# Performance work log

Hardware: AMD Instinct MI355X
Metric: run time of the kernel (lower is better)

## Reference

```python
import jax, jax.numpy as jnp
import numpy as np


def setup_inputs() -> dict:
    key = jax.random.key(0)
    k1, k2 = jax.random.split(key)
    B, C, H, W = 8, 64, 64, 64
    x = jax.random.normal(k1, (B, C, H, W), dtype=jnp.float32)
    stdv = 1.0 / np.sqrt(C)
    weight = jax.random.uniform(k2, (C, C), dtype=jnp.float32, minval=-stdv, maxval=stdv)
    return {"x": x, "weight": weight}


def reference(x, weight):
    B, C, H, W = x.shape
    N = H * W
    xf = x.reshape(B, C, N)            # [B, C, N]
    g_x = jnp.transpose(xf, (0, 2, 1))  # [B, N, C] (also theta_x)
    # f[b, i, j] = sum_c x[b, c, i] * x[b, c, j]
    f = jnp.einsum('bic,bcj->bij', g_x, xf)  # [B, N, N]
    adj = jax.nn.softmax(f, axis=-1)
    support = jnp.einsum('bnc,cd->bnd', g_x, weight)  # [B, N, C]
    y = jnp.einsum('bij,bjc->bic', adj, support)      # [B, N, C]
    y = jnp.transpose(y, (0, 2, 1)).reshape(B, C, H, W)
    return y + x
```

## Files before the change

### kernel.cpp

```cpp
#include <hip/hip_runtime.h>
#include <stdint.h>


#define NTOK 4096
#define CCH  64

typedef float v4f __attribute__((ext_vector_type(4)));
typedef __bf16 v8bf __attribute__((ext_vector_type(8)));
typedef unsigned short v8us __attribute__((ext_vector_type(8)));
typedef __fp16 v2fp __attribute__((ext_vector_type(2)));
typedef _Float16 v8h __attribute__((ext_vector_type(8)));

__device__ __forceinline__ unsigned short f2bf(float f) {
    union { float f; unsigned int u; } c; c.f = f;
    unsigned int r = c.u + 0x7fffu + ((c.u >> 16) & 1u);
    return (unsigned short)(r >> 16);
}

__device__ __forceinline__ v8bf ld8(const unsigned short* p) {
    union { v8us s; v8bf b; } u;
    u.s = *(const v8us*)p;
    return u.b;
}

__device__ __forceinline__ unsigned int pkbf(float a, float b) {
    union { float f; unsigned int u; } ua, ub; ua.f = a; ub.f = b;
    return __builtin_amdgcn_perm(ub.u, ua.u, 0x07060302u);
}

__device__ __forceinline__ float ex2(float x) {
#if __has_builtin(__builtin_amdgcn_exp2f)
    return __builtin_amdgcn_exp2f(x);
#else
    return exp2f(x);
#endif
}

__device__ __forceinline__ void gload_lds16(const void* g, void* l) {
    __builtin_amdgcn_global_load_lds(
        (const __attribute__((address_space(1))) unsigned int*)g,
        (__attribute__((address_space(3))) unsigned int*)l,
        16, 0, 0);
}

__global__ __launch_bounds__(256) void prep_kernel(
    const float* __restrict__ x,
    const float* __restrict__ w,
    unsigned short* __restrict__ xT,
    unsigned short* __restrict__ sT)
{
    __shared__ float Xf[64 * 65];

    const int tid  = threadIdx.x;
    const int lane = tid & 63;
    const int wv   = __builtin_amdgcn_readfirstlane(tid >> 6);
    const int b    = blockIdx.y;
    const int n0   = blockIdx.x * 64;

    const float* xb = x + (size_t)b * CCH * NTOK + n0 + lane;
    #pragma unroll
    for (int k = 0; k < 16; ++k) {
        const int c = wv * 16 + k;
        Xf[c * 65 + lane] = xb[(size_t)c * NTOK];
    }
    __syncthreads();

    {
        const int n  = tid >> 2;
        const int c0 = (tid & 3) * 16;
        unsigned int pk[8];
        #pragma unroll
        for (int k = 0; k < 8; ++k) {
            const float a = Xf[(c0 + 2 * k) * 65 + n];
            const float c2 = Xf[(c0 + 2 * k + 1) * 65 + n];
            pk[k] = (unsigned int)f2bf(a) | ((unsigned int)f2bf(c2) << 16);
        }
        unsigned short* xtr = xT + ((size_t)b * NTOK + n0 + n) * CCH + c0;
        *(uint4*)(xtr)     = *(uint4*)(pk);
        *(uint4*)(xtr + 8) = *(uint4*)(pk + 4);
    }

    float acc[16];
    #pragma unroll
    for (int d = 0; d < 16; ++d) acc[d] = 0.f;

    #pragma unroll 4
    for (int c = 0; c < 64; ++c) {
        const float xc = Xf[c * 65 + lane];
        const float* wr = w + c * 64 + wv * 16;
        #pragma unroll
        for (int d = 0; d < 16; ++d) acc[d] = fmaf(xc, wr[d], acc[d]);
    }
    unsigned short* stb = sT + (size_t)b * CCH * NTOK + n0 + lane;
    #pragma unroll
    for (int d = 0; d < 16; ++d)
        stb[(size_t)(wv * 16 + d) * NTOK] = f2bf(acc[d]);
}

__global__ __launch_bounds__(256, 4) void flash_kernel(
    const unsigned short* __restrict__ xT,
    const unsigned short* __restrict__ sT,
    unsigned short* __restrict__ part_o,
    float* __restrict__ part_l,
    int nchunk, int chunk_len)
{
    __shared__ __align__(16) unsigned short Kt[2][64 * 64];
    __shared__ __align__(16) unsigned short Vt[2][64 * 64];

    const int tid  = threadIdx.x;
    const int w    = tid >> 6;
    const int lane = tid & 63;
    const int quad = lane >> 4;
    const int l16  = lane & 15;
    const int b     = blockIdx.z;
    const int chunk = blockIdx.y;
    const int i0   = blockIdx.x * 128;
    const int irow = i0 + w * 32;
    const int jb   = chunk * chunk_len;

    const unsigned short* xTb = xT + (size_t)b * NTOK * CCH;
    const unsigned short* sTb = sT + (size_t)b * CCH * NTOK;

    const int srow = w * 8 + (lane >> 3);
    const int sc   = (lane & 7) ^ (lane >> 3);
    const int ksrow = 8 * ((srow & 12) >> 2) + 4 * ((srow >> 4) & 1) + (srow & 3);

    auto stage = [&](int j0, int bf) {
        unsigned short* kd = Kt[bf] + w * 512;
        unsigned short* vd = Vt[bf] + w * 512;
        gload_lds16(xTb + (size_t)(j0 + ksrow) * CCH + sc * 8,       kd);
        gload_lds16(xTb + (size_t)(j0 + 32 + ksrow) * CCH + sc * 8,  kd + 2048);
        gload_lds16(sTb + (size_t)srow * NTOK + j0 + sc * 8,        vd);
        gload_lds16(sTb + (size_t)(32 + srow) * NTOK + j0 + sc * 8, vd + 2048);
    };

    stage(jb, 0);

    v8bf aq0[2], aq1[2];
    #pragma unroll
    for (int m = 0; m < 2; ++m) {
        const unsigned short* qr = xTb + (size_t)(irow + m * 16 + l16) * CCH + quad * 8;
        aq0[m] = ld8(qr);
        aq1[m] = ld8(qr + 32);
    }

    const float L2E = 1.4426950408889634f;
    float negm2[2];
    #pragma unroll
    for (int m = 0; m < 2; ++m) {
        float msq = 0.f;
        #pragma unroll
        for (int i = 0; i < 8; ++i) {
            float e0 = (float)aq0[m][i], e1 = (float)aq1[m][i];
            msq = fmaf(e0, e0, msq);
            msq = fmaf(e1, e1, msq);
        }
        msq += __shfl_xor(msq, 16);
        msq += __shfl_xor(msq, 32);
        negm2[m] = -msq * L2E;
    }

    v4f o[2][4];
    #pragma unroll
    for (int m = 0; m < 2; ++m)
        #pragma unroll
        for (int ct = 0; ct < 4; ++ct) { o[m][ct][0]=0.f; o[m][ct][1]=0.f; o[m][ct][2]=0.f; o[m][ct][3]=0.f; }
    float rsum[2] = {0.f, 0.f};

    int cur = 0;
    for (int jj = 0; jj < chunk_len; jj += 64) {
        __syncthreads();
        if (jj + 64 < chunk_len)
            stage(jb + jj + 64, cur ^ 1);

        const unsigned short* Kc = Kt[cur];
        const unsigned short* Vc = Vt[cur];

        #pragma unroll
        for (int h = 0; h < 2; ++h) {
            uint2 pk[2][2];
            #pragma unroll
            for (int jtl = 0; jtl < 2; ++jtl) {
                const int krow = 32 * h + 16 * jtl + l16;
                const unsigned short* kb = Kc + krow * 64;
                const int c0 = quad ^ (krow & 7);
                v8bf bk0 = ld8(kb + c0 * 8);
                v8bf bk1 = ld8(kb + (c0 ^ 4) * 8);
                #pragma unroll
                for (int m = 0; m < 2; ++m) {
                    v4f z; z[0]=0.f; z[1]=0.f; z[2]=0.f; z[3]=0.f;
                    z = __builtin_amdgcn_mfma_f32_16x16x32_bf16(bk0, aq0[m], z, 0, 0, 0);
                    z = __builtin_amdgcn_mfma_f32_16x16x32_bf16(bk1, aq1[m], z, 0, 0, 0);
                    const float p0 = ex2(fmaf(z[0], L2E, negm2[m]));
                    const float p1 = ex2(fmaf(z[1], L2E, negm2[m]));
                    const float p2 = ex2(fmaf(z[2], L2E, negm2[m]));
                    const float p3 = ex2(fmaf(z[3], L2E, negm2[m]));
                    rsum[m] += (p0 + p1) + (p2 + p3);
                    pk[m][jtl].x = pkbf(p0, p1);
                    pk[m][jtl].y = pkbf(p2, p3);
                }
            }

            union { unsigned int u[4]; v8bf b; } pb[2];
            #pragma unroll
            for (int m = 0; m < 2; ++m) {
                pb[m].u[0] = pk[m][0].x; pb[m].u[1] = pk[m][0].y;
                pb[m].u[2] = pk[m][1].x; pb[m].u[3] = pk[m][1].y;
            }

            #pragma unroll
            for (int ct = 0; ct < 4; ++ct) {
                const int vrow = 16 * ct + l16;
                const unsigned short* vb = Vc + vrow * 64;
                const int cc = (4 * h + quad) ^ (vrow & 7);
                v8bf bv = ld8(vb + cc * 8);
                #pragma unroll
                for (int m = 0; m < 2; ++m)
                    o[m][ct] = __builtin_amdgcn_mfma_f32_16x16x32_bf16(bv, pb[m].b, o[m][ct], 0, 0, 0);
            }
        }
        cur ^= 1;
    }

    const size_t pbase = (size_t)(b * nchunk + chunk) * NTOK + irow;
    #pragma unroll
    for (int m = 0; m < 2; ++m) {
        float t = rsum[m];
        t += __shfl_xor(t, 16);
        t += __shfl_xor(t, 32);
        if (quad == 0) part_l[pbase + m * 16 + l16] = t;
    }
    unsigned short* po = part_o + pbase * 64;
    #pragma unroll
    for (int m = 0; m < 2; ++m)
        #pragma unroll
        for (int ct = 0; ct < 4; ++ct) {
            union { struct { v2fp a, b; } h; uint2 u; } cv;
            cv.h.a = __builtin_amdgcn_cvt_pkrtz(o[m][ct][0], o[m][ct][1]);
            cv.h.b = __builtin_amdgcn_cvt_pkrtz(o[m][ct][2], o[m][ct][3]);
            *(uint2*)(po + (size_t)(m * 16 + l16) * 64 + ct * 16 + quad * 4) = cv.u;
        }
}

__global__ __launch_bounds__(256) void combine_kernel(
    const unsigned short* __restrict__ part_o,
    const float* __restrict__ part_l,
    const float* __restrict__ x,
    float* __restrict__ out,
    int nchunk)
{
    __shared__ float Of[64 * 65];
    const int tid = threadIdx.x;
    const int b = blockIdx.y;
    const int i0 = blockIdx.x * 64;
    const int row = tid >> 2;
    const int seg = tid & 3;

    float acc[16];
    #pragma unroll
    for (int k = 0; k < 16; ++k) acc[k] = 0.f;
    float lt = 0.f;

    auto body = [&](int ch) {
        const size_t base = (size_t)(b * nchunk + ch) * NTOK + i0 + row;
        lt += part_l[base];
        const unsigned short* po = part_o + base * 64 + seg * 16;
        v8h a = *(const v8h*)(po);
        v8h c2 = *(const v8h*)(po + 8);
        #pragma unroll
        for (int k = 0; k < 8; ++k) {
            acc[k]     += (float)a[k];
            acc[8 + k] += (float)c2[k];
        }
    };
    if (nchunk == 4) { body(0); body(1); body(2); body(3); }
    else { for (int ch = 0; ch < nchunk; ++ch) body(ch); }

    const float inv = 1.f / lt;
    #pragma unroll
    for (int k = 0; k < 16; ++k) Of[row * 65 + seg * 16 + k] = acc[k] * inv;
    __syncthreads();

    const int c    = tid >> 2;
    const int part = tid & 3;
    const float* xrow = x   + ((size_t)b * CCH + c) * NTOK + i0 + part * 16;
    float*       orow = out + ((size_t)b * CCH + c) * NTOK + i0 + part * 16;
    #pragma unroll
    for (int i4 = 0; i4 < 4; ++i4) {
        float4 xv = *(const float4*)(xrow + i4 * 4);
        float4 ov;
        ov.x = Of[(part * 16 + i4 * 4 + 0) * 65 + c] + xv.x;
        ov.y = Of[(part * 16 + i4 * 4 + 1) * 65 + c] + xv.y;
        ov.z = Of[(part * 16 + i4 * 4 + 2) * 65 + c] + xv.z;
        ov.w = Of[(part * 16 + i4 * 4 + 3) * 65 + c] + xv.w;
        *(float4*)(orow + i4 * 4) = ov;
    }
}

extern "C" void kernel_launch(void* const* d_in, const int* in_sizes, int n_in,
                              void* d_out, int out_size, void* d_ws, size_t ws_size,
                              hipStream_t stream) {
    const float* x = (const float*)d_in[0];
    const float* w = (const float*)d_in[1];
    float* out = (float*)d_out;

    const size_t xT_elems = (size_t)8 * NTOK * CCH;
    unsigned short* xT = (unsigned short*)d_ws;
    unsigned short* sT = xT + xT_elems;
    char* rest = (char*)d_ws + 2 * xT_elems * sizeof(unsigned short);

    int KS = 4;
    while (KS > 1) {
        size_t need = 2 * xT_elems * sizeof(unsigned short)
                    + (size_t)KS * ((size_t)8 * NTOK * CCH * 2 + (size_t)8 * NTOK * 4);
        if (need <= ws_size) break;
        KS >>= 1;
    }
    unsigned short* part_o = (unsigned short*)rest;
    float* part_l = (float*)(rest + (size_t)KS * 8 * NTOK * CCH * 2);

    dim3 gp(64, 8);
    prep_kernel<<<gp, 256, 0, stream>>>(x, w, xT, sT);
    dim3 gf(32, KS, 8);
    flash_kernel<<<gf, 256, 0, stream>>>(xT, sT, part_o, part_l, KS, NTOK / KS);
    dim3 gc(64, 8);
    combine_kernel<<<gc, 256, 0, stream>>>(part_o, part_l, x, out, KS);
}
```

Before: 119.3 us.

## Fuse split-K combine into flash kernel via last-block atomic counter

Removes the separate combine kernel launch. Each flash block increments a per-tile atomic counter after writing its partials, and the last-arriving chunk block reduces all partials, normalises, adds the residual and writes the output. The shared memory for the K/V tiles is reused for the transpose buffer. The counters are zeroed in the prep kernel. This saves a launch and its tail, but the reduction now runs only on the last blocks, which can lengthen the flash kernel's tail.

```diff
diff --git a/kernel.cpp b/kernel.cpp
--- a/kernel.cpp
+++ b/kernel.cpp
@@ -47,7 +47,8 @@
     const float* __restrict__ x,
     const float* __restrict__ w,
     unsigned short* __restrict__ xT,
-    unsigned short* __restrict__ sT)
+    unsigned short* __restrict__ sT,
+    int* __restrict__ cnt)
 {
     __shared__ float Xf[64 * 65];
 
@@ -57,6 +58,9 @@
     const int b    = blockIdx.y;
     const int n0   = blockIdx.x * 64;
 
+    if (blockIdx.x == 0 && blockIdx.y == 0)
+        cnt[tid] = 0;
+
     const float* xb = x + (size_t)b * CCH * NTOK + n0 + lane;
     #pragma unroll
     for (int k = 0; k < 16; ++k) {
@@ -102,10 +106,15 @@
     const unsigned short* __restrict__ sT,
     unsigned short* __restrict__ part_o,
     float* __restrict__ part_l,
+    const float* __restrict__ x,
+    float* __restrict__ out,
+    int* __restrict__ cnt,
     int nchunk, int chunk_len)
 {
-    __shared__ __align__(16) unsigned short Kt[2][64 * 64];
-    __shared__ __align__(16) unsigned short Vt[2][64 * 64];
+    __shared__ __align__(16) unsigned char smem[32768];
+    __shared__ int s_last;
+    unsigned short* KT = (unsigned short*)smem;
+    unsigned short* VT = KT + 2 * 4096;
 
     const int tid  = threadIdx.x;
     const int w    = tid >> 6;
@@ -126,8 +135,8 @@
     const int ksrow = 8 * ((srow & 12) >> 2) + 4 * ((srow >> 4) & 1) + (srow & 3);
 
     auto stage = [&](int j0, int bf) {
-        unsigned short* kd = Kt[bf] + w * 512;
-        unsigned short* vd = Vt[bf] + w * 512;
+        unsigned short* kd = KT + bf * 4096 + w * 512;
+        unsigned short* vd = VT + bf * 4096 + w * 512;
         gload_lds16(xTb + (size_t)(j0 + ksrow) * CCH + sc * 8,       kd);
         gload_lds16(xTb + (size_t)(j0 + 32 + ksrow) * CCH + sc * 8,  kd + 2048);
         gload_lds16(sTb + (size_t)srow * NTOK + j0 + sc * 8,        vd);
@@ -173,8 +182,8 @@
         if (jj + 64 < chunk_len)
             stage(jb + jj + 64, cur ^ 1);
 
-        const unsigned short* Kc = Kt[cur];
-        const unsigned short* Vc = Vt[cur];
+        const unsigned short* Kc = KT + cur * 4096;
+        const unsigned short* Vc = VT + cur * 4096;
 
         #pragma unroll
         for (int h = 0; h < 2; ++h) {
@@ -240,60 +249,65 @@
             cv.h.b = __builtin_amdgcn_cvt_pkrtz(o[m][ct][2], o[m][ct][3]);
             *(uint2*)(po + (size_t)(m * 16 + l16) * 64 + ct * 16 + quad * 4) = cv.u;
         }
-}
-
-__global__ __launch_bounds__(256) void combine_kernel(
-    const unsigned short* __restrict__ part_o,
-    const float* __restrict__ part_l,
-    const float* __restrict__ x,
-    float* __restrict__ out,
-    int nchunk)
-{
-    __shared__ float Of[64 * 65];
-    const int tid = threadIdx.x;
-    const int b = blockIdx.y;
-    const int i0 = blockIdx.x * 64;
+
+    __threadfence();
+    __syncthreads();
+    if (tid == 0)
+        s_last = (atomicAdd(&cnt[b * 32 + blockIdx.x], 1) == nchunk - 1);
+    __syncthreads();
+    if (!s_last) return;
+    __threadfence();
+
+    float* Of = (float*)smem;
     const int row = tid >> 2;
     const int seg = tid & 3;
-
-    float acc[16];
-    #pragma unroll
-    for (int k = 0; k < 16; ++k) acc[k] = 0.f;
-    float lt = 0.f;
-
-    auto body = [&](int ch) {
-        const size_t base = (size_t)(b * nchunk + ch) * NTOK + i0 + row;
-        lt += part_l[base];
-        const unsigned short* po = part_o + base * 64 + seg * 16;
-        v8h a = *(const v8h*)(po);
-        v8h c2 = *(const v8h*)(po + 8);
-        #pragma unroll
-        for (int k = 0; k < 8; ++k) {
-            acc[k]     += (float)a[k];
-            acc[8 + k] += (float)c2[k];
-        }
-    };
-    if (nchunk == 4) { body(0); body(1); body(2); body(3); }
-    else { for (int ch = 0; ch < nchunk; ++ch) body(ch); }
-
-    const float inv = 1.f / lt;
-    #pragma unroll
-    for (int k = 0; k < 16; ++k) Of[row * 65 + seg * 16 + k] = acc[k] * inv;
-    __syncthreads();
-
     const int c    = tid >> 2;
     const int part = tid & 3;
-    const float* xrow = x   + ((size_t)b * CCH + c) * NTOK + i0 + part * 16;
-    float*       orow = out + ((size_t)b * CCH + c) * NTOK + i0 + part * 16;
-    #pragma unroll
-    for (int i4 = 0; i4 < 4; ++i4) {
-        float4 xv = *(const float4*)(xrow + i4 * 4);
-        float4 ov;
-        ov.x = Of[(part * 16 + i4 * 4 + 0) * 65 + c] + xv.x;
-        ov.y = Of[(part * 16 + i4 * 4 + 1) * 65 + c] + xv.y;
-        ov.z = Of[(part * 16 + i4 * 4 + 2) * 65 + c] + xv.z;
-        ov.w = Of[(part * 16 + i4 * 4 + 3) * 65 + c] + xv.w;
-        *(float4*)(orow + i4 * 4) = ov;
+    const float* xb2  = x   + (size_t)b * CCH * NTOK;
+    float*       outb = out + (size_t)b * CCH * NTOK;
+
+    #pragma unroll
+    for (int g = 0; g < 2; ++g) {
+        const int r0 = i0 + g * 64;
+
+        float acc[16];
+        #pragma unroll
+        for (int k = 0; k < 16; ++k) acc[k] = 0.f;
+        float lt = 0.f;
+
+        auto body = [&](int ch) {
+            const size_t base = (size_t)(b * nchunk + ch) * NTOK + r0 + row;
+            lt += part_l[base];
+            const unsigned short* pp = part_o + base * 64 + seg * 16;
+            v8h a  = *(const v8h*)(pp);
+            v8h c2 = *(const v8h*)(pp + 8);
+            #pragma unroll
+            for (int k = 0; k < 8; ++k) {
+                acc[k]     += (float)a[k];
+                acc[8 + k] += (float)c2[k];
+            }
+        };
+        if (nchunk == 4) { body(0); body(1); body(2); body(3); }
+        else { for (int ch = 0; ch < nchunk; ++ch) body(ch); }
+
+        const float inv = 1.f / lt;
+        #pragma unroll
+        for (int k = 0; k < 16; ++k) Of[row * 65 + seg * 16 + k] = acc[k] * inv;
+        __syncthreads();
+
+        const float* xrow = xb2  + (size_t)c * NTOK + r0 + part * 16;
+        float*       orow = outb + (size_t)c * NTOK + r0 + part * 16;
+        #pragma unroll
+        for (int i4 = 0; i4 < 4; ++i4) {
+            float4 xv = *(const float4*)(xrow + i4 * 4);
+            float4 ov;
+            ov.x = Of[(part * 16 + i4 * 4 + 0) * 65 + c] + xv.x;
+            ov.y = Of[(part * 16 + i4 * 4 + 1) * 65 + c] + xv.y;
+            ov.z = Of[(part * 16 + i4 * 4 + 2) * 65 + c] + xv.z;
+            ov.w = Of[(part * 16 + i4 * 4 + 3) * 65 + c] + xv.w;
+            *(float4*)(orow + i4 * 4) = ov;
+        }
+        __syncthreads();
     }
 }
 
@@ -312,17 +326,17 @@
     int KS = 4;
     while (KS > 1) {
         size_t need = 2 * xT_elems * sizeof(unsigned short)
-                    + (size_t)KS * ((size_t)8 * NTOK * CCH * 2 + (size_t)8 * NTOK * 4);
+                    + (size_t)KS * ((size_t)8 * NTOK * CCH * 2 + (size_t)8 * NTOK * 4)
+                    + 1024;
         if (need <= ws_size) break;
         KS >>= 1;
     }
     unsigned short* part_o = (unsigned short*)rest;
     float* part_l = (float*)(rest + (size_t)KS * 8 * NTOK * CCH * 2);
+    int* cnt = (int*)((char*)part_l + (size_t)KS * 8 * NTOK * 4);
 
     dim3 gp(64, 8);
-    prep_kernel<<<gp, 256, 0, stream>>>(x, w, xT, sT);
+    prep_kernel<<<gp, 256, 0, stream>>>(x, w, xT, sT, cnt);
     dim3 gf(32, KS, 8);
-    flash_kernel<<<gf, 256, 0, stream>>>(xT, sT, part_o, part_l, KS, NTOK / KS);
-    dim3 gc(64, 8);
-    combine_kernel<<<gc, 256, 0, stream>>>(part_o, part_l, x, out, KS);
-}
+    flash_kernel<<<gf, 256, 0, stream>>>(xT, sT, part_o, part_l, x, out, cnt, KS, NTOK / KS);
+}
```

After: 283.2 us. 137% more time.

## Double flash block to 512 threads and interleave batch across linear grid

Applied to the files above, without the earlier changes.

The flash kernel now runs 8 waves per block, covering 256 query rows per block. Each wave stages one K row-group and one V row-group instead of two, so the shared K/V tiles are reused by twice as many waves. All three kernels switch to 1D grids with batch in the low bits of blockIdx.x, which spreads batches across XCDs and changes L2 locality. The larger blocks with launch bounds (512,4) may constrain registers and halve the block count.

```diff
diff --git a/kernel.cpp b/kernel.cpp
--- a/kernel.cpp
+++ b/kernel.cpp
@@ -54,8 +54,8 @@
     const int tid  = threadIdx.x;
     const int lane = tid & 63;
     const int wv   = __builtin_amdgcn_readfirstlane(tid >> 6);
-    const int b    = blockIdx.y;
-    const int n0   = blockIdx.x * 64;
+    const int b    = blockIdx.x & 7;
+    const int n0   = (blockIdx.x >> 3) * 64;
 
     const float* xb = x + (size_t)b * CCH * NTOK + n0 + lane;
     #pragma unroll
@@ -97,7 +97,7 @@
         stb[(size_t)(wv * 16 + d) * NTOK] = f2bf(acc[d]);
 }
 
-__global__ __launch_bounds__(256, 4) void flash_kernel(
+__global__ __launch_bounds__(512, 4) void flash_kernel(
     const unsigned short* __restrict__ xT,
     const unsigned short* __restrict__ sT,
     unsigned short* __restrict__ part_o,
@@ -112,26 +112,26 @@
     const int lane = tid & 63;
     const int quad = lane >> 4;
     const int l16  = lane & 15;
-    const int b     = blockIdx.z;
-    const int chunk = blockIdx.y;
-    const int i0   = blockIdx.x * 128;
-    const int irow = i0 + w * 32;
-    const int jb   = chunk * chunk_len;
+
+    const int L     = blockIdx.x;
+    const int b     = L & 7;
+    const int t     = L >> 3;
+    const int i0    = (t & 15) * 256;
+    const int chunk = t >> 4;
+    const int irow  = i0 + w * 32;
+    const int jb    = chunk * chunk_len;
 
     const unsigned short* xTb = xT + (size_t)b * NTOK * CCH;
     const unsigned short* sTb = sT + (size_t)b * CCH * NTOK;
 
     const int srow = w * 8 + (lane >> 3);
     const int sc   = (lane & 7) ^ (lane >> 3);
-    const int ksrow = 8 * ((srow & 12) >> 2) + 4 * ((srow >> 4) & 1) + (srow & 3);
+    const int ksrow = 32 * (srow >> 5) + 8 * ((srow & 12) >> 2)
+                    + 4 * ((srow >> 4) & 1) + (srow & 3);
 
     auto stage = [&](int j0, int bf) {
-        unsigned short* kd = Kt[bf] + w * 512;
-        unsigned short* vd = Vt[bf] + w * 512;
-        gload_lds16(xTb + (size_t)(j0 + ksrow) * CCH + sc * 8,       kd);
-        gload_lds16(xTb + (size_t)(j0 + 32 + ksrow) * CCH + sc * 8,  kd + 2048);
-        gload_lds16(sTb + (size_t)srow * NTOK + j0 + sc * 8,        vd);
-        gload_lds16(sTb + (size_t)(32 + srow) * NTOK + j0 + sc * 8, vd + 2048);
+        gload_lds16(xTb + (size_t)(j0 + ksrow) * CCH + sc * 8, Kt[bf] + w * 512);
+        gload_lds16(sTb + (size_t)srow * NTOK + j0 + sc * 8,   Vt[bf] + w * 512);
     };
 
     stage(jb, 0);
@@ -225,10 +225,10 @@
     const size_t pbase = (size_t)(b * nchunk + chunk) * NTOK + irow;
     #pragma unroll
     for (int m = 0; m < 2; ++m) {
-        float t = rsum[m];
-        t += __shfl_xor(t, 16);
-        t += __shfl_xor(t, 32);
-        if (quad == 0) part_l[pbase + m * 16 + l16] = t;
+        float t2 = rsum[m];
+        t2 += __shfl_xor(t2, 16);
+        t2 += __shfl_xor(t2, 32);
+        if (quad == 0) part_l[pbase + m * 16 + l16] = t2;
     }
     unsigned short* po = part_o + pbase * 64;
     #pragma unroll
@@ -251,8 +251,8 @@
 {
     __shared__ float Of[64 * 65];
     const int tid = threadIdx.x;
-    const int b = blockIdx.y;
-    const int i0 = blockIdx.x * 64;
+    const int b  = blockIdx.x & 7;
+    const int i0 = (blockIdx.x >> 3) * 64;
     const int row = tid >> 2;
     const int seg = tid & 3;
 
@@ -319,10 +319,7 @@
     unsigned short* part_o = (unsigned short*)rest;
     float* part_l = (float*)(rest + (size_t)KS * 8 * NTOK * CCH * 2);
 
-    dim3 gp(64, 8);
-    prep_kernel<<<gp, 256, 0, stream>>>(x, w, xT, sT);
-    dim3 gf(32, KS, 8);
-    flash_kernel<<<gf, 256, 0, stream>>>(xT, sT, part_o, part_l, KS, NTOK / KS);
-    dim3 gc(64, 8);
-    combine_kernel<<<gc, 256, 0, stream>>>(part_o, part_l, x, out, KS);
-}
+    prep_kernel<<<512, 256, 0, stream>>>(x, w, xT, sT);
+    flash_kernel<<<128 * KS, 512, 0, stream>>>(xT, sT, part_o, part_l, KS, NTOK / KS);
+    combine_kernel<<<512, 256, 0, stream>>>(part_o, part_l, x, out, KS);
+}
```

New measurement: 122.5 us. +2.6%, slower.
